# Optimization experiments

Hardware: AMD Instinct MI355X
Metric: run time of the kernel (lower is better)

The kernel has to match this reference:

```python
import jax, jax.numpy as jnp
import numpy as np

CONF_THRESH = 0.3
NMS_THRESH = 0.5
TOP_K = 64
VAR = (0.1, 0.2)  # standard SSD decode variances


def setup_inputs() -> dict:
    key = jax.random.key(0)
    k1, k2, k3 = jax.random.split(key, 3)
    B, A, C = 16, 16384, 81
    loc = jax.random.normal(k1, (B, A, 4), jnp.float32)
    conf = jax.random.normal(k2, (B, A, C), jnp.float32)
    anchors = jax.random.uniform(k3, (A, 4), jnp.float32)  # cxcywh in [0,1]
    return {"loc": loc, "conf": conf, "anchors": anchors}


def _decode(loc, anchors):
    # SSD-style decode: loc [A,4] offsets, anchors [A,4] cxcywh -> corners [A,4]
    cxcy = anchors[:, :2] + loc[:, :2] * VAR[0] * anchors[:, 2:]
    wh = anchors[:, 2:] * jnp.exp(loc[:, 2:] * VAR[1])
    tl = cxcy - wh * 0.5
    return jnp.concatenate([tl, tl + wh], axis=1)


def _iou(box, boxes):
    # box [4], boxes [A,4] in corner format
    tl = jnp.maximum(box[:2], boxes[:, :2])
    br = jnp.minimum(box[2:], boxes[:, 2:])
    wh = jnp.clip(br - tl, 0.0)
    inter = wh[:, 0] * wh[:, 1]
    a1 = (box[2] - box[0]) * (box[3] - box[1])
    a2 = (boxes[:, 2] - boxes[:, 0]) * (boxes[:, 3] - boxes[:, 1])
    return inter / (a1 + a2 - inter)


def _nms(boxes, scores):
    # greedy NMS for one (batch, class) lane; boxes [A,4], scores [A]
    s0 = jnp.where(scores > CONF_THRESH, scores, -1.0)

    def step(s, _):
        i = jnp.argmax(s)
        sc = s[i]
        box = boxes[i]
        keep = sc > 0.0  # -1 means masked/suppressed; valid scores > conf_thresh > 0
        supp = jnp.where(_iou(box, boxes) > NMS_THRESH, -1.0, s).at[i].set(-1.0)
        s_next = jnp.where(keep, supp, s)
        row = jnp.where(keep, jnp.concatenate([sc[None], box]),
                        jnp.zeros((5,), s.dtype))
        return s_next, row

    _, rows = jax.lax.scan(step, s0, None, length=TOP_K)
    return rows  # [TOP_K, 5] = (score, x1, y1, x2, y2), zero-padded


def reference(loc, conf, anchors):
    conf = jax.nn.sigmoid(conf)                      # [B,A,C]
    boxes = jax.vmap(_decode, in_axes=(0, None))(loc, anchors)  # [B,A,4]
    scores = jnp.swapaxes(conf, 1, 2)                # [B,C,A]
    per_class = jax.vmap(_nms, in_axes=(None, 0))    # over classes
    out = jax.vmap(per_class)(boxes, scores)         # [B,C,TOP_K,5]
    return out
```

## Files before the change

### kernel.cpp

```cpp
#include <hip/hip_runtime.h>
#include <math.h>

constexpr int B_N  = 16;
constexpr int A_N  = 16384;
constexpr int C_N  = 81;
constexpr int TOPK = 64;
constexpr int DNT  = 256;
constexpr int NBINS = 232;
constexpr int CAP   = 512;
constexpr unsigned BIN_BASE = 0x3E99u;
constexpr int SNT = 256;
constexpr int BC_N = B_N * C_N;
constexpr int GCAP_MAX = 2048;

#define IOU_HALF_EXACT 0x1.000001p-1

constexpr int TA   = 64;
constexpr int TNT  = 256;
constexpr int TILE_ELEMS = TA * C_N;
constexpr int TILE_F4    = TILE_ELEMS / 4;

__global__ __launch_bounds__(DNT) void decode_kernel(const float4* __restrict__ loc,
                                                     const float4* __restrict__ anch,
                                                     float4* __restrict__ boxes) {
    int i = blockIdx.x * DNT + threadIdx.x;
    int a = i & (A_N - 1);
    float4 l  = loc[i];
    float4 an = anch[a];
    float cx = an.x + (l.x * 0.1f) * an.z;
    float cy = an.y + (l.y * 0.1f) * an.w;
    float w  = an.z * expf(l.z * 0.2f);
    float h  = an.w * expf(l.w * 0.2f);
    float x1 = cx - w * 0.5f;
    float y1 = cy - h * 0.5f;
    boxes[i] = make_float4(x1, y1, x1 + w, y1 + h);
}

__global__ __launch_bounds__(TNT) void sigT_kernel(const float* __restrict__ conf,
                                                   float* __restrict__ scoresT) {
    __shared__ float4 tile4[TILE_F4];
    float* tile = (float*)tile4;

    const int a0 = blockIdx.x * TA;
    const int b  = blockIdx.y;
    const int t  = threadIdx.x;

    const float4* src = (const float4*)(conf + ((size_t)b * A_N + a0) * C_N);
#pragma unroll
    for (int i = 0; i < (TILE_F4 + TNT - 1) / TNT; ++i) {
        int idx4 = i * TNT + t;
        if (idx4 < TILE_F4) {
            float4 x = src[idx4];
            float4 v;
            v.x = 1.0f / (1.0f + expf(-x.x));
            v.y = 1.0f / (1.0f + expf(-x.y));
            v.z = 1.0f / (1.0f + expf(-x.z));
            v.w = 1.0f / (1.0f + expf(-x.w));
            tile4[idx4] = v;
        }
    }
    __syncthreads();
    float* dst = scoresT + (size_t)b * C_N * A_N + a0;
#pragma unroll
    for (int i = 0; i < (TILE_F4 + TNT - 1) / TNT; ++i) {
        int idx4 = i * TNT + t;
        if (idx4 < TILE_F4) {
            int cc  = idx4 >> 4;
            int al4 = idx4 & 15;
            int e   = al4 * 4 * C_N + cc;
            float4 v;
            v.x = tile[e];
            v.y = tile[e + C_N];
            v.z = tile[e + 2 * C_N];
            v.w = tile[e + 3 * C_N];
            ((float4*)(dst + (size_t)cc * A_N))[al4] = v;
        }
    }
}

__device__ __forceinline__ void sort_gather_scan64(
        unsigned long long* cand, float4* cbox, int C, int lane,
        const float4* __restrict__ bptr, float* __restrict__ optr,
        float& rx1, float& ry1, float& rx2, float& ry2, float& rar,
        int& acc, int& kout) {
    unsigned long long key[8];
#pragma unroll
    for (int r = 0; r < 8; ++r) {
        int sidx = r * 64 + lane;
        key[r] = (sidx < C) ? cand[sidx] : 0ull;
    }
#pragma unroll
    for (int k = 2; k <= CAP; k <<= 1) {
#pragma unroll
        for (int j = k >> 1; j > 0; j >>= 1) {
            if (j >= 64) {
                int jr = j >> 6;
#pragma unroll
                for (int r = 0; r < 8; ++r) {
                    int rp = r ^ jr;
                    if (rp > r) {
                        int e = r * 64 + lane;
                        bool up = ((e & k) == 0);
                        unsigned long long va = key[r], vb = key[rp];
                        bool sw = up ? (va < vb) : (va > vb);
                        if (sw) { key[r] = vb; key[rp] = va; }
                    }
                }
            } else {
#pragma unroll
                for (int r = 0; r < 8; ++r) {
                    int e = r * 64 + lane;
                    bool up    = ((e & k) == 0);
                    bool isLow = ((lane & j) == 0);
                    unsigned long long va = key[r];
                    unsigned long long vb = __shfl_xor(va, j, 64);
                    bool keepMax = (up == isLow);
                    key[r] = keepMax ? (va > vb ? va : vb) : (va < vb ? va : vb);
                }
            }
        }
    }
    __syncthreads();
#pragma unroll
    for (int r = 0; r < 8; ++r) cand[r * 64 + lane] = key[r];
    __syncthreads();
#pragma unroll
    for (int r = 0; r < 8; ++r) {
        int e = r * 64 + lane;
        if (e < C) cbox[e] = bptr[(int)(~(unsigned)cand[e])];
    }
    __syncthreads();

    int ts = 0;
    unsigned long long k0 = cand[0];
    float4 cb = cbox[0];
    while (ts < C) {
        unsigned long long nk = 0ull;
        float4 nb = cb;
        if (ts + 1 < C) { nk = cand[ts + 1]; nb = cbox[ts + 1]; }
        float sc = __uint_as_float((unsigned)(k0 >> 32));
        float ca = (cb.z - cb.x) * (cb.w - cb.y);
        bool over = false;
        if (lane < acc) {
            float tlx = fmaxf(rx1, cb.x);
            float tly = fmaxf(ry1, cb.y);
            float brx = fminf(rx2, cb.z);
            float bry = fminf(ry2, cb.w);
            float iw  = fmaxf(brx - tlx, 0.0f);
            float ih  = fmaxf(bry - tly, 0.0f);
            float inter = iw * ih;
            float iou = inter / (rar + ca - inter);
            over = iou > 0.5f;
        }
        if (!__any(over)) {
            if (lane == acc) { rx1 = cb.x; ry1 = cb.y; rx2 = cb.z; ry2 = cb.w; rar = ca; }
            if (lane == 0) {
                float* o = optr + (size_t)kout * 5;
                o[0] = sc; o[1] = cb.x; o[2] = cb.y; o[3] = cb.z; o[4] = cb.w;
            }
            acc++; kout++;
            if (acc == TOPK) break;
        }
        ++ts; k0 = nk; cb = nb;
    }
}

__device__ __forceinline__ void suppress_mask(
        unsigned& aliveM, const float4& bb, float bar,
        const float4 (&breg)[8], const float (&careg)[8]) {
#pragma unroll
    for (int r = 0; r < 8; ++r) {
        float tlx = fmaxf(bb.x, breg[r].x);
        float tly = fmaxf(bb.y, breg[r].y);
        float brx = fminf(bb.z, breg[r].z);
        float bry = fminf(bb.w, breg[r].w);
        float iw  = fmaxf(brx - tlx, 0.0f);
        float ih  = fmaxf(bry - tly, 0.0f);
        float inter = iw * ih;
        float den = bar + careg[r] - inter;
        if ((double)inter > (double)den * IOU_HALF_EXACT) aliveM &= ~(1u << r);
    }
}

__device__ __forceinline__ void sort_mask_accept(
        unsigned long long (&key)[8], int C, int lane,
        unsigned long long* cand, float4* cbox, float4* abox, float* aar,
        const float4* __restrict__ bptr, float* __restrict__ optr,
        int& acc, int& kout) {
#pragma unroll
    for (int k = 2; k <= CAP; k <<= 1) {
#pragma unroll
        for (int j = k >> 1; j > 0; j >>= 1) {
            if (j >= 64) {
                int jr = j >> 6;
#pragma unroll
                for (int r = 0; r < 8; ++r) {
                    int rp = r ^ jr;
                    if (rp > r) {
                        int e = r * 64 + lane;
                        bool up = ((e & k) == 0);
                        unsigned long long va = key[r], vb = key[rp];
                        bool sw = up ? (va < vb) : (va > vb);
                        if (sw) { key[r] = vb; key[rp] = va; }
                    }
                }
            } else {
#pragma unroll
                for (int r = 0; r < 8; ++r) {
                    int e = r * 64 + lane;
                    bool up    = ((e & k) == 0);
                    bool isLow = ((lane & j) == 0);
                    unsigned long long va = key[r];
                    unsigned long long vb = __shfl_xor(va, j, 64);
                    bool keepMax = (up == isLow);
                    key[r] = keepMax ? (va > vb ? va : vb) : (va < vb ? va : vb);
                }
            }
        }
    }
    __syncthreads();
#pragma unroll
    for (int r = 0; r < 8; ++r) cand[r * 64 + lane] = key[r];
    __syncthreads();

    float4 breg[8];
    float  careg[8];
#pragma unroll
    for (int r = 0; r < 8; ++r) {
        int e = r * 64 + lane;
        float4 v = make_float4(0.f, 0.f, 0.f, 0.f);
        if (e < C) { v = bptr[(int)(~(unsigned)key[r])]; cbox[e] = v; }
        breg[r]  = v;
        careg[r] = (v.z - v.x) * (v.w - v.y);
    }
    __syncthreads();

    unsigned aliveM = 0;
#pragma unroll
    for (int r = 0; r < 8; ++r)
        if (r * 64 + lane < C) aliveM |= (1u << r);

    for (int a = 0; a < acc; ++a)
        suppress_mask(aliveM, abox[a], aar[a], breg, careg);

    int rStart = 0;
    while (acc < TOPK) {
        int estar = -1;
        for (int r = rStart; r < 8; ++r) {
            unsigned long long m = __ballot((aliveM >> r) & 1);
            if (m != 0ull) { estar = r * 64 + __builtin_ctzll(m); rStart = r; break; }
        }
        if (estar < 0) break;

        unsigned long long k0 = cand[estar];
        float4 bb = cbox[estar];
        float sc  = __uint_as_float((unsigned)(k0 >> 32));
        float bar = (bb.z - bb.x) * (bb.w - bb.y);

        if (lane == 0) {
            float* o = optr + (size_t)kout * 5;
            o[0] = sc; o[1] = bb.x; o[2] = bb.y; o[3] = bb.z; o[4] = bb.w;
            abox[acc] = bb; aar[acc] = bar;
        }
        acc++; kout++;

        suppress_mask(aliveM, bb, bar, breg, careg);
    }
}

__global__ __launch_bounds__(SNT) void select_kernel(
        const float* __restrict__ scoresT,
        unsigned long long* __restrict__ g_cand,
        int* __restrict__ g_hist,
        int gcap) {
    __shared__ int hist[NBINS];
    __shared__ int cur[NBINS];
    __shared__ int sfx[NBINS + 1];

    const int bc = blockIdx.x;
    const int t  = threadIdx.x;

    for (int i = t; i < NBINS; i += SNT) { hist[i] = 0; cur[i] = 0; }
    __syncthreads();

    const float4* sptr = (const float4*)(scoresT + (size_t)bc * A_N);

    for (int i = 0; i < A_N / 4 / SNT; ++i) {
        float4 s4 = sptr[t + SNT * i];
        float s[4] = {s4.x, s4.y, s4.z, s4.w};
#pragma unroll
        for (int q = 0; q < 4; ++q) {
            if (s[q] > 0.3f) {
                unsigned u = __float_as_uint(s[q]);
                int bin = (int)(u >> 16) - (int)BIN_BASE;
                bin = bin < 0 ? 0 : (bin > NBINS - 1 ? NBINS - 1 : bin);
                atomicAdd(&hist[bin], 1);
            }
        }
    }
    __syncthreads();

    for (int i = t; i < NBINS; i += SNT) g_hist[bc * NBINS + i] = hist[i];
    if (t == 0) {
        sfx[NBINS] = 0;
        for (int b = NBINS - 1; b >= 0; --b) sfx[b] = sfx[b + 1] + hist[b];
    }
    __syncthreads();

    unsigned long long* gc = g_cand + (size_t)bc * gcap;
    for (int i = 0; i < A_N / 4 / SNT; ++i) {
        float4 s4 = sptr[t + SNT * i];
        float s[4] = {s4.x, s4.y, s4.z, s4.w};
#pragma unroll
        for (int q = 0; q < 4; ++q) {
            if (s[q] > 0.3f) {
                unsigned u = __float_as_uint(s[q]);
                int bin = (int)(u >> 16) - (int)BIN_BASE;
                bin = bin < 0 ? 0 : (bin > NBINS - 1 ? NBINS - 1 : bin);
                int base = sfx[bin + 1];
                if (base < gcap) {
                    int g = base + atomicAdd(&cur[bin], 1);
                    if (g < gcap) {
                        unsigned a = (unsigned)(4 * (t + SNT * i) + q);
                        gc[g] = ((unsigned long long)u << 32) | (unsigned)(~a);
                    }
                }
            }
        }
    }
}

__global__ __launch_bounds__(64, 2) void nms_banded_kernel(
        const float* __restrict__ scoresT,
        const float4* __restrict__ boxes,
        const unsigned long long* __restrict__ g_cand,
        const int* __restrict__ g_hist,
        float* __restrict__ out,
        int gcap) {
    __shared__ int hist[NBINS];
    __shared__ int sfx[NBINS + 1];
    __shared__ unsigned long long cand[CAP];
    __shared__ float4 cbox[CAP];
    __shared__ float4 abox[TOPK];
    __shared__ float  aar[TOPK];
    __shared__ int s_cnt;

    const int bc   = blockIdx.x;
    const int b    = bc / C_N;
    const int lane = threadIdx.x;

    const float4* sptr = (const float4*)(scoresT + (size_t)bc * A_N);
    const float4* bptr = boxes + (size_t)b * A_N;
    const unsigned long long* gc = g_cand + (size_t)bc * gcap;
    float* optr = out + (size_t)bc * TOPK * 5;

    for (int i = lane; i < NBINS; i += 64) hist[i] = g_hist[bc * NBINS + i];
    __syncthreads();
    if (lane == 0) {
        sfx[NBINS] = 0;
        for (int bn = NBINS - 1; bn >= 0; --bn) sfx[bn] = sfx[bn + 1] + hist[bn];
    }
    __syncthreads();

    int acc = 0, kout = 0;
    int bin_hi = NBINS;

    while (acc < TOPK) {
        int lo = bin_hi, tot = 0;
        while (lo > 0) {
            int cnt = hist[lo - 1];
            if (tot + cnt > CAP) {
                if (tot == 0) { lo--; }
                break;
            }
            tot += cnt; lo--;
        }
        const int bin_lo = lo;
        if (bin_lo == bin_hi) break;

        const int start = sfx[bin_hi];
        int C = sfx[bin_lo] - start;
        if (C > CAP) C = CAP;

        if (C > 0) {
            if (start + C <= gcap) {
                unsigned long long key[8];
#pragma unroll
                for (int r = 0; r < 8; ++r) {
                    int e = r * 64 + lane;
                    key[r] = (e < C) ? gc[start + e] : 0ull;
                }
                sort_mask_accept(key, C, lane, cand, cbox, abox, aar,
                                 bptr, optr, acc, kout);
            } else {
                if (lane == 0) s_cnt = 0;
                __syncthreads();
                for (int i = 0; i < A_N / 4 / 64; ++i) {
                    float4 s4 = sptr[lane + 64 * i];
                    float s[4] = {s4.x, s4.y, s4.z, s4.w};
#pragma unroll
                    for (int q = 0; q < 4; ++q) {
                        if (s[q] > 0.3f) {
                            unsigned u = __float_as_uint(s[q]);
                            int bin = (int)(u >> 16) - (int)BIN_BASE;
                            bin = bin < 0 ? 0 : (bin > NBINS - 1 ? NBINS - 1 : bin);
                            if (bin >= bin_lo && bin < bin_hi) {
                                int slot = atomicAdd(&s_cnt, 1);
                                if (slot < CAP) {
                                    unsigned a = (unsigned)(4 * (lane + 64 * i) + q);
                                    cand[slot] = ((unsigned long long)u << 32) | (unsigned)(~a);
                                }
                            }
                        }
                    }
                }
                __syncthreads();
                int Cr = s_cnt; if (Cr > CAP) Cr = CAP;
                if (Cr > 0) {
                    unsigned long long key[8];
#pragma unroll
                    for (int r = 0; r < 8; ++r) {
                        int e = r * 64 + lane;
                        key[r] = (e < Cr) ? cand[e] : 0ull;
                    }
                    sort_mask_accept(key, Cr, lane, cand, cbox, abox, aar,
                                     bptr, optr, acc, kout);
                }
            }
        }
        bin_hi = bin_lo;
    }

    {
        float* o  = optr + (size_t)kout * 5;
        int   rem = (TOPK - kout) * 5;
        for (int i = lane; i < rem; i += 64) o[i] = 0.0f;
    }
}

__global__ __launch_bounds__(SNT, 4) void select_nms_fused(
        const float* __restrict__ scoresT,
        const float4* __restrict__ boxes,
        float* __restrict__ out) {
    __shared__ int hist[NBINS];
    __shared__ unsigned long long cand[CAP];
    __shared__ float4 cbox[CAP];
    __shared__ int s_cnt, s_acc, s_kout;

    const int bc   = blockIdx.x;
    const int b    = bc / C_N;
    const int t    = threadIdx.x;
    const int lane = t & 63;
    const int wv   = t >> 6;

    for (int i = t; i < NBINS; i += SNT) hist[i] = 0;
    if (t == 0) { s_acc = 0; s_kout = 0; }
    __syncthreads();

    const float4* sptr = (const float4*)(scoresT + (size_t)bc * A_N);
    const float4* bptr = boxes + (size_t)b * A_N;
    float* optr = out + (size_t)bc * TOPK * 5;

    for (int i = 0; i < A_N / 4 / SNT; ++i) {
        float4 s4 = sptr[t + SNT * i];
        float s[4] = {s4.x, s4.y, s4.z, s4.w};
#pragma unroll
        for (int q = 0; q < 4; ++q) {
            if (s[q] > 0.3f) {
                unsigned u = __float_as_uint(s[q]);
                int bin = (int)(u >> 16) - (int)BIN_BASE;
                bin = bin < 0 ? 0 : (bin > NBINS - 1 ? NBINS - 1 : bin);
                atomicAdd(&hist[bin], 1);
            }
        }
    }
    __syncthreads();

    float rx1 = 0.f, ry1 = 0.f, rx2 = 0.f, ry2 = 0.f, rar = 0.f;
    int acc = 0, kout = 0;

    int bin_hi = NBINS;
    for (;;) {
        int lo = bin_hi, tot = 0;
        while (lo > 0) {
            int cnt = hist[lo - 1];
            if (tot + cnt > CAP) { if (tot == 0) { lo--; } break; }
            tot += cnt; lo--;
        }
        const int bin_lo = lo;
        if (bin_lo == bin_hi) break;
        if (t == 0) s_cnt = 0;
        __syncthreads();

        for (int i = 0; i < A_N / 4 / SNT; ++i) {
            float4 s4 = sptr[t + SNT * i];
            float s[4] = {s4.x, s4.y, s4.z, s4.w};
#pragma unroll
            for (int q = 0; q < 4; ++q) {
                if (s[q] > 0.3f) {
                    unsigned u = __float_as_uint(s[q]);
                    int bin = (int)(u >> 16) - (int)BIN_BASE;
                    bin = bin < 0 ? 0 : (bin > NBINS - 1 ? NBINS - 1 : bin);
                    if (bin >= bin_lo && bin < bin_hi) {
                        int slot = atomicAdd(&s_cnt, 1);
                        if (slot < CAP) {
                            unsigned a = (unsigned)(4 * (t + SNT * i) + q);
                            cand[slot] = ((unsigned long long)u << 32) | (unsigned)(~a);
                        }
                    }
                }
            }
        }
        __syncthreads();
        int C = s_cnt; if (C > CAP) C = CAP;

        if (C > 0) {
            if (wv == 0) {
                unsigned long long key[8];
#pragma unroll
                for (int r = 0; r < 8; ++r) {
                    int sidx = r * 64 + lane;
                    key[r] = (sidx < C) ? cand[sidx] : 0ull;
                }
#pragma unroll
                for (int k = 2; k <= CAP; k <<= 1) {
#pragma unroll
                    for (int j = k >> 1; j > 0; j >>= 1) {
                        if (j >= 64) {
                            int jr = j >> 6;
#pragma unroll
                            for (int r = 0; r < 8; ++r) {
                                int rp = r ^ jr;
                                if (rp > r) {
                                    int e = r * 64 + lane;
                                    bool up = ((e & k) == 0);
                                    unsigned long long va = key[r], vb = key[rp];
                                    bool sw = up ? (va < vb) : (va > vb);
                                    if (sw) { key[r] = vb; key[rp] = va; }
                                }
                            }
                        } else {
#pragma unroll
                            for (int r = 0; r < 8; ++r) {
                                int e = r * 64 + lane;
                                bool up    = ((e & k) == 0);
                                bool isLow = ((lane & j) == 0);
                                unsigned long long va = key[r];
                                unsigned long long vb = __shfl_xor(va, j, 64);
                                bool keepMax = (up == isLow);
                                key[r] = keepMax ? (va > vb ? va : vb)
                                                 : (va < vb ? va : vb);
                            }
                        }
                    }
                }
#pragma unroll
                for (int r = 0; r < 8; ++r) cand[r * 64 + lane] = key[r];
            }
            __syncthreads();

            for (int e = t; e < CAP; e += SNT)
                if (e < C) cbox[e] = bptr[(int)(~(unsigned)cand[e])];
            __syncthreads();

            if (wv == 0) {
                int ts = 0;
                unsigned long long k0 = cand[0];
                float4 cb = cbox[0];
                while (ts < C) {
                    unsigned long long nk = 0ull;
                    float4 nb = cb;
                    if (ts + 1 < C) { nk = cand[ts + 1]; nb = cbox[ts + 1]; }
                    float sc = __uint_as_float((unsigned)(k0 >> 32));
                    float ca = (cb.z - cb.x) * (cb.w - cb.y);
                    bool over = false;
                    if (lane < acc) {
                        float tlx = fmaxf(rx1, cb.x);
                        float tly = fmaxf(ry1, cb.y);
                        float brx = fminf(rx2, cb.z);
                        float bry = fminf(ry2, cb.w);
                        float iw  = fmaxf(brx - tlx, 0.0f);
                        float ih  = fmaxf(bry - tly, 0.0f);
                        float inter = iw * ih;
                        float iou = inter / (rar + ca - inter);
                        over = iou > 0.5f;
                    }
                    if (!__any(over)) {
                        if (lane == acc) { rx1 = cb.x; ry1 = cb.y; rx2 = cb.z; ry2 = cb.w; rar = ca; }
                        if (lane == 0) {
                            float* o = optr + (size_t)kout * 5;
                            o[0] = sc; o[1] = cb.x; o[2] = cb.y; o[3] = cb.z; o[4] = cb.w;
                        }
                        acc++; kout++;
                        if (acc == TOPK) break;
                    }
                    ++ts; k0 = nk; cb = nb;
                }
                if (lane == 0) { s_acc = acc; s_kout = kout; }
            }
            __syncthreads();
            if (s_acc >= TOPK) break;
        }
        bin_hi = bin_lo;
    }

    {
        const int ko = s_kout;
        float* o  = optr + (size_t)ko * 5;
        int   rem = (TOPK - ko) * 5;
        for (int i = t; i < rem; i += SNT) o[i] = 0.0f;
    }
}

__global__ __launch_bounds__(64, 4) void nms_fallback(const float* __restrict__ conf,
                                                      const float4* __restrict__ boxes,
                                                      float* __restrict__ out) {
    __shared__ int hist[NBINS];
    __shared__ unsigned long long cand[CAP];
    __shared__ float4 cbox[CAP];
    __shared__ int s_cnt;

    const int c    = blockIdx.x;
    const int b    = blockIdx.y;
    const int lane = threadIdx.x;

    const float4* bptr = boxes + (size_t)b * A_N;
    const float*  cptr = conf + (size_t)b * A_N * C_N + c;
    float* optr = out + (size_t)(b * C_N + c) * TOPK * 5;

    for (int i = lane; i < NBINS; i += 64) hist[i] = 0;
    __syncthreads();
    for (int i = 0; i < A_N / 256; ++i) {
        int a0 = 4 * (lane + 64 * i);
#pragma unroll
        for (int q = 0; q < 4; ++q) {
            float x = cptr[(size_t)(a0 + q) * C_N];
            float s = 1.0f / (1.0f + expf(-x));
            if (s > 0.3f) {
                unsigned u = __float_as_uint(s);
                int bin = (int)(u >> 16) - (int)BIN_BASE;
                bin = bin < 0 ? 0 : (bin > NBINS - 1 ? NBINS - 1 : bin);
                atomicAdd(&hist[bin], 1);
            }
        }
    }
    __syncthreads();

    float rx1 = 0.f, ry1 = 0.f, rx2 = 0.f, ry2 = 0.f, rar = 0.f;
    int acc = 0, kout = 0;
    int bin_hi = NBINS;
    for (;;) {
        int lo = bin_hi, tot = 0;
        while (lo > 0) {
            int cnt = hist[lo - 1];
            if (tot + cnt > CAP) { if (tot == 0) { lo--; } break; }
            tot += cnt; lo--;
        }
        const int bin_lo = lo;
        if (bin_lo == bin_hi) break;
        if (lane == 0) s_cnt = 0;
        __syncthreads();
        for (int i = 0; i < A_N / 256; ++i) {
            int a0 = 4 * (lane + 64 * i);
#pragma unroll
            for (int q = 0; q < 4; ++q) {
                float x = cptr[(size_t)(a0 + q) * C_N];
                float s = 1.0f / (1.0f + expf(-x));
                if (s > 0.3f) {
                    unsigned u = __float_as_uint(s);
                    int bin = (int)(u >> 16) - (int)BIN_BASE;
                    bin = bin < 0 ? 0 : (bin > NBINS - 1 ? NBINS - 1 : bin);
                    if (bin >= bin_lo && bin < bin_hi) {
                        int slot = atomicAdd(&s_cnt, 1);
                        if (slot < CAP)
                            cand[slot] = ((unsigned long long)u << 32) | (unsigned)(~(unsigned)(a0 + q));
                    }
                }
            }
        }
        __syncthreads();
        int C = s_cnt; if (C > CAP) C = CAP;
        if (C > 0)
            sort_gather_scan64(cand, cbox, C, lane, bptr, optr,
                               rx1, ry1, rx2, ry2, rar, acc, kout);
        if (acc == TOPK) break;
        bin_hi = bin_lo;
    }
    {
        float* o  = optr + (size_t)kout * 5;
        int   rem = (TOPK - kout) * 5;
        for (int i = lane; i < rem; i += 64) o[i] = 0.0f;
    }
}

extern "C" void kernel_launch(void* const* d_in, const int* in_sizes, int n_in,
                              void* d_out, int out_size, void* d_ws, size_t ws_size,
                              hipStream_t stream) {
    const float* loc     = (const float*)d_in[0];
    const float* conf    = (const float*)d_in[1];
    const float* anchors = (const float*)d_in[2];
    float* out = (float*)d_out;

    const size_t boxes_bytes  = (size_t)B_N * A_N * sizeof(float4);
    const size_t scores_bytes = (size_t)B_N * C_N * A_N * sizeof(float);
    const size_t hist_bytes   = (size_t)BC_N * NBINS * sizeof(int);
    const size_t fixed_bytes  = boxes_bytes + scores_bytes + hist_bytes;
    const size_t min_cand     = (size_t)BC_N * CAP * sizeof(unsigned long long);

    float4* boxes = (float4*)d_ws;

    decode_kernel<<<(B_N * A_N) / DNT, DNT, 0, stream>>>(
        (const float4*)loc, (const float4*)anchors, boxes);

    if (ws_size >= fixed_bytes + min_cand) {
        size_t avail = ws_size - fixed_bytes;
        int gcap = (int)(avail / ((size_t)BC_N * sizeof(unsigned long long)));
        if (gcap > GCAP_MAX) gcap = GCAP_MAX;

        char* p = (char*)d_ws + boxes_bytes;
        float* scoresT = (float*)p;                 p += scores_bytes;
        int* g_hist = (int*)p;                      p += hist_bytes;
        unsigned long long* g_cand = (unsigned long long*)p;

        sigT_kernel<<<dim3(A_N / TA, B_N), TNT, 0, stream>>>(conf, scoresT);
        select_kernel<<<dim3(BC_N), SNT, 0, stream>>>(scoresT, g_cand, g_hist, gcap);
        nms_banded_kernel<<<dim3(BC_N), 64, 0, stream>>>(scoresT, boxes, g_cand,
                                                         g_hist, out, gcap);
    } else if (ws_size >= boxes_bytes + scores_bytes) {
        float* scoresT = (float*)((char*)d_ws + boxes_bytes);
        sigT_kernel<<<dim3(A_N / TA, B_N), TNT, 0, stream>>>(conf, scoresT);
        select_nms_fused<<<dim3(BC_N), SNT, 0, stream>>>(scoresT, boxes, out);
    } else {
        nms_fallback<<<dim3(C_N, B_N), 64, 0, stream>>>(conf, boxes, out);
    }
}
```

Measured before the change: 268.3 us.

## Prefilter later NMS bands against accepted boxes before sorting, and scan hist with wave ops

For later score bands, candidates are first suppressed against already-accepted boxes and compacted, so only survivors are sorted. Small survivor sets (at most 64) go through an in-register wave bitonic sort and a direct greedy loop. The suppression loop also exits early once every candidate is dead. The serial suffix sum and band search are replaced with wave shuffle and ballot operations, and GCAP_MAX is doubled to 4096 so the fallback rescan of scores is needed less often. This adds code complexity and extra synchronisation, and raises global candidate buffer size.

```diff
diff --git a/kernel.cpp b/kernel.cpp
--- a/kernel.cpp
+++ b/kernel.cpp
@@ -11,7 +11,7 @@
 constexpr unsigned BIN_BASE = 0x3E99u;
 constexpr int SNT = 256;
 constexpr int BC_N = B_N * C_N;
-constexpr int GCAP_MAX = 2048;
+constexpr int GCAP_MAX = 4096;
 
 #define IOU_HALF_EXACT 0x1.000001p-1
 
@@ -240,8 +240,10 @@
     for (int r = 0; r < 8; ++r)
         if (r * 64 + lane < C) aliveM |= (1u << r);
 
-    for (int a = 0; a < acc; ++a)
+    for (int a = 0; a < acc; ++a) {
         suppress_mask(aliveM, abox[a], aar[a], breg, careg);
+        if (!__any(aliveM != 0u)) break;
+    }
 
     int rStart = 0;
     while (acc < TOPK) {
@@ -337,8 +339,7 @@
         const int* __restrict__ g_hist,
         float* __restrict__ out,
         int gcap) {
-    __shared__ int hist[NBINS];
-    __shared__ int sfx[NBINS + 1];
+    __shared__ int sfx[257];
     __shared__ unsigned long long cand[CAP];
     __shared__ float4 cbox[CAP];
     __shared__ float4 abox[TOPK];
@@ -354,54 +355,61 @@
     const unsigned long long* gc = g_cand + (size_t)bc * gcap;
     float* optr = out + (size_t)bc * TOPK * 5;
 
-    for (int i = lane; i < NBINS; i += 64) hist[i] = g_hist[bc * NBINS + i];
-    __syncthreads();
-    if (lane == 0) {
-        sfx[NBINS] = 0;
-        for (int bn = NBINS - 1; bn >= 0; --bn) sfx[bn] = sfx[bn + 1] + hist[bn];
-    }
+    const int* gh = g_hist + bc * NBINS;
+    int4 hv = make_int4(0, 0, 0, 0);
+    if (lane < NBINS / 4) hv = ((const int4*)gh)[lane];
+    int s = hv.x + hv.y + hv.z + hv.w;
+#pragma unroll
+    for (int j = 1; j < 64; j <<= 1) {
+        int tv = __shfl_down(s, j, 64);
+        if (lane + j < 64) s += tv;
+    }
+    sfx[4 * lane + 0] = s;
+    sfx[4 * lane + 1] = s - hv.x;
+    sfx[4 * lane + 2] = s - hv.x - hv.y;
+    sfx[4 * lane + 3] = s - hv.x - hv.y - hv.z;
+    if (lane == 0) sfx[256] = 0;
     __syncthreads();
 
     int acc = 0, kout = 0;
     int bin_hi = NBINS;
 
-    while (acc < TOPK) {
-        int lo = bin_hi, tot = 0;
-        while (lo > 0) {
-            int cnt = hist[lo - 1];
-            if (tot + cnt > CAP) {
-                if (tot == 0) { lo--; }
-                break;
-            }
-            tot += cnt; lo--;
-        }
-        const int bin_lo = lo;
-        if (bin_lo == bin_hi) break;
-
-        const int start = sfx[bin_hi];
-        int C = sfx[bin_lo] - start;
-        if (C > CAP) C = CAP;
+    while (acc < TOPK && bin_hi > 0) {
+        const int base = sfx[bin_hi];
+        int lostar = bin_hi;
+        for (int off = 0; off < bin_hi; off += 64) {
+            int l = bin_hi - 1 - off - lane;
+            bool ok = (l >= 0) && (sfx[l] - base <= CAP);
+            unsigned long long m = __ballot(ok);
+            if (m == 0ull) break;
+            unsigned long long inv = ~m;
+            int nok = (inv == 0ull) ? 64 : __builtin_ctzll(inv);
+            lostar = bin_hi - off - nok;
+            if (nok < 64) break;
+        }
+        int bin_lo, C;
+        if (lostar < bin_hi) { bin_lo = lostar; C = sfx[bin_lo] - base; }
+        else { bin_lo = bin_hi - 1; C = sfx[bin_lo] - base; if (C > CAP) C = CAP; }
 
         if (C > 0) {
-            if (start + C <= gcap) {
-                unsigned long long key[8];
+            unsigned long long key[8];
+            int Cb = C;
+            if (base + C <= gcap) {
 #pragma unroll
                 for (int r = 0; r < 8; ++r) {
                     int e = r * 64 + lane;
-                    key[r] = (e < C) ? gc[start + e] : 0ull;
-                }
-                sort_mask_accept(key, C, lane, cand, cbox, abox, aar,
-                                 bptr, optr, acc, kout);
+                    key[r] = (e < Cb) ? gc[base + e] : 0ull;
+                }
             } else {
                 if (lane == 0) s_cnt = 0;
                 __syncthreads();
                 for (int i = 0; i < A_N / 4 / 64; ++i) {
                     float4 s4 = sptr[lane + 64 * i];
-                    float s[4] = {s4.x, s4.y, s4.z, s4.w};
+                    float sv[4] = {s4.x, s4.y, s4.z, s4.w};
 #pragma unroll
                     for (int q = 0; q < 4; ++q) {
-                        if (s[q] > 0.3f) {
-                            unsigned u = __float_as_uint(s[q]);
+                        if (sv[q] > 0.3f) {
+                            unsigned u = __float_as_uint(sv[q]);
                             int bin = (int)(u >> 16) - (int)BIN_BASE;
                             bin = bin < 0 ? 0 : (bin > NBINS - 1 ? NBINS - 1 : bin);
                             if (bin >= bin_lo && bin < bin_hi) {
@@ -415,16 +423,115 @@
                     }
                 }
                 __syncthreads();
-                int Cr = s_cnt; if (Cr > CAP) Cr = CAP;
-                if (Cr > 0) {
-                    unsigned long long key[8];
+                Cb = s_cnt; if (Cb > CAP) Cb = CAP;
+#pragma unroll
+                for (int r = 0; r < 8; ++r) {
+                    int e = r * 64 + lane;
+                    key[r] = (e < Cb) ? cand[e] : 0ull;
+                }
+                __syncthreads();
+            }
+
+            if (Cb > 0) {
+                if (acc == 0) {
+                    sort_mask_accept(key, Cb, lane, cand, cbox, abox, aar,
+                                     bptr, optr, acc, kout);
+                } else {
+                    float4 breg[8];
+                    float  careg[8];
 #pragma unroll
                     for (int r = 0; r < 8; ++r) {
                         int e = r * 64 + lane;
-                        key[r] = (e < Cr) ? cand[e] : 0ull;
-                    }
-                    sort_mask_accept(key, Cr, lane, cand, cbox, abox, aar,
-                                     bptr, optr, acc, kout);
+                        float4 v = make_float4(0.f, 0.f, 0.f, 0.f);
+                        if (e < Cb) v = bptr[(int)(~(unsigned)key[r])];
+                        else        key[r] = 0ull;
+                        breg[r]  = v;
+                        careg[r] = (v.z - v.x) * (v.w - v.y);
+                    }
+                    unsigned aliveM = 0;
+#pragma unroll
+                    for (int r = 0; r < 8; ++r)
+                        if (r * 64 + lane < Cb) aliveM |= (1u << r);
+
+                    for (int a = 0; a < acc; ++a) {
+                        suppress_mask(aliveM, abox[a], aar[a], breg, careg);
+                        if (!__any(aliveM != 0u)) break;
+                    }
+
+                    int cb2 = 0;
+#pragma unroll
+                    for (int r = 0; r < 8; ++r) {
+                        unsigned long long m = __ballot((aliveM >> r) & 1u);
+                        int pre = (int)__popcll(m & ((1ull << lane) - 1ull));
+                        if ((aliveM >> r) & 1u) {
+                            cand[cb2 + pre] = key[r];
+                            cbox[cb2 + pre] = breg[r];
+                        }
+                        cb2 += (int)__popcll(m);
+                    }
+                    const int C1 = cb2;
+                    __syncthreads();
+
+                    if (C1 > 64) {
+                        unsigned long long k2[8];
+#pragma unroll
+                        for (int r = 0; r < 8; ++r) {
+                            int e = r * 64 + lane;
+                            k2[r] = (e < C1) ? cand[e] : 0ull;
+                        }
+                        __syncthreads();
+                        sort_mask_accept(k2, C1, lane, cand, cbox, abox, aar,
+                                         bptr, optr, acc, kout);
+                    } else if (C1 > 0) {
+                        unsigned long long k0 = (lane < C1) ? cand[lane] : 0ull;
+#pragma unroll
+                        for (int k = 2; k <= 64; k <<= 1) {
+#pragma unroll
+                            for (int j = k >> 1; j > 0; j >>= 1) {
+                                bool up    = ((lane & k) == 0);
+                                bool isLow = ((lane & j) == 0);
+                                unsigned long long vb = __shfl_xor(k0, j, 64);
+                                bool keepMax = (up == isLow);
+                                k0 = keepMax ? (k0 > vb ? k0 : vb)
+                                             : (k0 < vb ? k0 : vb);
+                            }
+                        }
+                        cand[lane] = k0;
+                        float4 mb = make_float4(0.f, 0.f, 0.f, 0.f);
+                        if (lane < C1) mb = bptr[(int)(~(unsigned)k0)];
+                        cbox[lane] = mb;
+                        float mar = (mb.z - mb.x) * (mb.w - mb.y);
+                        __syncthreads();
+
+                        bool alive = (lane < C1);
+                        while (acc < TOPK) {
+                            unsigned long long m = __ballot(alive);
+                            if (m == 0ull) break;
+                            int e = __builtin_ctzll(m);
+                            unsigned long long kk = cand[e];
+                            float4 wb = cbox[e];
+                            float war = (wb.z - wb.x) * (wb.w - wb.y);
+                            if (lane == 0) {
+                                float* o = optr + (size_t)kout * 5;
+                                o[0] = __uint_as_float((unsigned)(kk >> 32));
+                                o[1] = wb.x; o[2] = wb.y; o[3] = wb.z; o[4] = wb.w;
+                                abox[acc] = wb; aar[acc] = war;
+                            }
+                            acc++; kout++;
+                            if (alive) {
+                                float tlx = fmaxf(wb.x, mb.x);
+                                float tly = fmaxf(wb.y, mb.y);
+                                float brx = fminf(wb.z, mb.z);
+                                float bry = fminf(wb.w, mb.w);
+                                float iw  = fmaxf(brx - tlx, 0.0f);
+                                float ih  = fmaxf(bry - tly, 0.0f);
+                                float inter = iw * ih;
+                                float den = war + mar - inter;
+                                if ((double)inter > (double)den * IOU_HALF_EXACT)
+                                    alive = false;
+                            }
+                        }
+                    }
                 }
             }
         }
```

New measurement: 280.5 us. +4.5%, slower.
